# Optimization experiments

Hardware: AMD Instinct MI355X
Metric: run time of the kernel (lower is better)

## Reference

```python
import jax, jax.numpy as jnp
import numpy as np

B, S, D, H = 2, 2048, 1024, 16
HD = D // H  # 64

def setup_inputs() -> dict:
    key = jax.random.key(0)
    ks = jax.random.split(key, 11)
    s = 1.0 / np.sqrt(D)
    inp = {
        "q": jax.random.normal(ks[0], (B, S, D), jnp.float32),
        "k": jax.random.normal(ks[1], (B, S, D), jnp.float32),
        "v": jax.random.normal(ks[2], (B, S, D), jnp.float32),
        "Wq": jax.random.normal(ks[3], (D, D), jnp.float32) * s,
        "bq": jnp.zeros((D,), jnp.float32),
        "Wk": jax.random.normal(ks[4], (D, D), jnp.float32) * s,
        "bk": jnp.zeros((D,), jnp.float32),
        "Wv": jax.random.normal(ks[5], (D, D), jnp.float32) * s,
        "bv": jnp.zeros((D,), jnp.float32),
        "Wo": jax.random.normal(ks[6], (D, D), jnp.float32) * s,
        "bo": jnp.zeros((D,), jnp.float32),
    }
    return inp

def _split_heads(x):
    # [B,S,D] -> [B,H,S,HD]
    b = x.shape[0]
    return x.reshape(b, -1, H, HD).transpose(0, 2, 1, 3)

def reference(q, k, v, Wq, bq, Wk, bk, Wv, bv, Wo, bo):
    qh = _split_heads(q @ Wq.T + bq)
    kh = _split_heads(k @ Wk.T + bk)
    vh = _split_heads(v @ Wv.T + bv)
    scale = 1.0 / jnp.sqrt(jnp.asarray(HD, qh.dtype))
    scores = jnp.einsum("bhqd,bhkd->bhqk", qh, kh) * scale  # [B,H,S,S]
    atten = jax.nn.softmax(scores, axis=-1)  # dropout is eval-mode no-op
    ctx = jnp.einsum("bhqk,bhkd->bhqd", atten, vh)
    out = ctx.transpose(0, 2, 1, 3).reshape(q.shape[0], -1, D)
    return out @ Wo.T + bo, atten
```

## Files before the change

kernel.cpp:

```cpp
#include <hip/hip_runtime.h>
#include <cstdint>

#define B_ 2
#define S_ 2048
#define D_ 1024
#define H_ 16

typedef __bf16 bf16x8 __attribute__((ext_vector_type(8)));
typedef float  f32x4  __attribute__((ext_vector_type(4)));

__device__ __forceinline__ void g2l16(const void* g, void* l) {
  auto* gp = reinterpret_cast<const __attribute__((address_space(1))) uint32_t*>(
      reinterpret_cast<uintptr_t>(g));
  auto* lp = reinterpret_cast<__attribute__((address_space(3))) uint32_t*>(
      reinterpret_cast<uintptr_t>(l));
  __builtin_amdgcn_global_load_lds(gp, lp, 16, 0, 0);
}

__device__ __forceinline__ float exp2_hw(float x) {
#if __has_builtin(__builtin_amdgcn_exp2f)
  return __builtin_amdgcn_exp2f(x);
#else
  return __exp2f(x);
#endif
}

struct CvtArgs {
  const float* s[7];
  __bf16* d[7];
  int n[7];
};

__global__ __launch_bounds__(256) void k_cvt(CvtArgs a) {
  int t = blockIdx.y;
  long i = (long)blockIdx.x * blockDim.x + threadIdx.x;
  long base = i * 8;
  if (base >= a.n[t]) return;
  const float4* sp = (const float4*)(a.s[t] + base);
  float4 x = sp[0], y = sp[1];
  bf16x8 o;
  o[0] = (__bf16)x.x; o[1] = (__bf16)x.y; o[2] = (__bf16)x.z; o[3] = (__bf16)x.w;
  o[4] = (__bf16)y.x; o[5] = (__bf16)y.y; o[6] = (__bf16)y.z; o[7] = (__bf16)y.w;
  *(bf16x8*)(a.d[t] + base) = o;
}

__global__ __launch_bounds__(256, 3) void k_proj(
    const __bf16* __restrict__ Xq, const __bf16* __restrict__ Xk, const __bf16* __restrict__ Xv,
    const __bf16* __restrict__ Wq, const __bf16* __restrict__ Wk, const __bf16* __restrict__ Wv,
    const float* __restrict__ bq, const float* __restrict__ bk, const float* __restrict__ bv,
    __bf16* __restrict__ Oq, __bf16* __restrict__ Ok, __bf16* __restrict__ Ov)
{
  int z = blockIdx.z;
  const __bf16* X = (z == 0) ? Xq : (z == 1) ? Xk : Xv;
  const __bf16* W = (z == 0) ? Wq : (z == 1) ? Wk : Wv;
  const float* bias = (z == 0) ? bq : (z == 1) ? bk : bv;
  __bf16* O = (z == 0) ? Oq : (z == 1) ? Ok : Ov;
  float scale = (z == 0) ? 0.180336880111183f : 1.0f;

  __shared__ bf16x8 As[3][512];
  __shared__ bf16x8 Bs[3][512];

  int t = threadIdx.x, lane = t & 63, w = t >> 6;
  int l15 = lane & 15, l4 = lane >> 4;
  int wr = w >> 1, wc = w & 1;
  int m0 = blockIdx.y * 128, n0 = blockIdx.x * 128;

  int srow = t >> 2, sc = t & 3;
  int ldsoff = __builtin_amdgcn_readfirstlane(w * 1024);
  const __bf16* Xs = X + (size_t)(m0 + srow) * 1024 + sc * 8;
  const __bf16* Wsp = W + (size_t)(n0 + srow) * 1024 + sc * 8;

#define PSTAGE(buf, kt)                                                        \
  {                                                                            \
    _Pragma("unroll")                                                          \
    for (int i = 0; i < 2; ++i) {                                              \
      int lo = __builtin_amdgcn_readfirstlane(i * 4096 + ldsoff);              \
      g2l16(Xs + (size_t)i * 64 * 1024 + (kt) * 32, (char*)As[buf] + lo);      \
      g2l16(Wsp + (size_t)i * 64 * 1024 + (kt) * 32, (char*)Bs[buf] + lo);     \
    }                                                                          \
  }

  f32x4 acc[4][4] = {};

  PSTAGE(0, 0)
  PSTAGE(1, 1)
  asm volatile("s_waitcnt vmcnt(4)" ::: "memory");
  __builtin_amdgcn_s_barrier();
  __builtin_amdgcn_sched_barrier(0);

  int ring = 0;
  for (int kt = 0; kt < 32; ++kt) {
    int cur = ring;
    int rp2 = (ring == 0) ? 2 : ring - 1;
    if (kt + 2 < 32) PSTAGE(rp2, kt + 2)
    __builtin_amdgcn_sched_barrier(0);

    bf16x8 af[4], bfr[4];
#pragma unroll
    for (int i = 0; i < 4; ++i) af[i] = As[cur][(wr * 64 + i * 16 + l15) * 4 + l4];
#pragma unroll
    for (int j = 0; j < 4; ++j) bfr[j] = Bs[cur][(wc * 64 + j * 16 + l15) * 4 + l4];
#pragma unroll
    for (int i = 0; i < 4; ++i)
#pragma unroll
      for (int j = 0; j < 4; ++j)
        acc[i][j] = __builtin_amdgcn_mfma_f32_16x16x32_bf16(af[i], bfr[j], acc[i][j], 0, 0, 0);

    if (kt < 30) {
      asm volatile("s_waitcnt vmcnt(4)" ::: "memory");
      __builtin_amdgcn_s_barrier();
      __builtin_amdgcn_sched_barrier(0);
    } else if (kt == 30) {
      asm volatile("s_waitcnt vmcnt(0)" ::: "memory");
      __builtin_amdgcn_s_barrier();
      __builtin_amdgcn_sched_barrier(0);
    }
    ring = (ring == 2) ? 0 : ring + 1;
  }
#undef PSTAGE

#pragma unroll
  for (int j = 0; j < 4; ++j) {
    int col = n0 + wc * 64 + j * 16 + l15;
    float bv_ = bias[col];
    int h = col >> 6, hd = col & 63;
#pragma unroll
    for (int i = 0; i < 4; ++i) {
#pragma unroll
      for (int r = 0; r < 4; ++r) {
        int row = m0 + wr * 64 + i * 16 + l4 * 4 + r;
        int b = row >> 11, ss = row & 2047;
        float val = (acc[i][j][r] + bv_) * scale;
        O[(((size_t)b * H_ + h) * S_ + ss) * 64 + hd] = (__bf16)val;
      }
    }
  }
}

__global__ __launch_bounds__(256) void k_trans(const __bf16* __restrict__ Vh,
                                               __bf16* __restrict__ VhT)
{
  __shared__ __bf16 Tt[64][72];
  int bid = blockIdx.x;
  int bh = bid >> 5, st = bid & 31;
  int t = threadIdx.x;
  int sr = t >> 2, dc = (t & 3) * 16;
  const __bf16* src = Vh + (((size_t)bh * S_) + st * 64 + sr) * 64 + dc;
  *(bf16x8*)&Tt[sr][dc] = *(const bf16x8*)src;
  *(bf16x8*)&Tt[sr][dc + 8] = *(const bf16x8*)(src + 8);
  __syncthreads();
  int dr = t >> 2, s0 = (t & 3) * 16;
  bf16x8 o0, o1;
#pragma unroll
  for (int ii = 0; ii < 8; ++ii) { o0[ii] = Tt[s0 + ii][dr]; o1[ii] = Tt[s0 + 8 + ii][dr]; }
  __bf16* dst = VhT + ((size_t)bh * 64 + dr) * S_ + st * 64 + s0;
  *(bf16x8*)dst = o0;
  *(bf16x8*)(dst + 8) = o1;
}

__global__ __launch_bounds__(512, 4) void k_attn(
    const __bf16* __restrict__ Qh, const __bf16* __restrict__ Kh,
    const __bf16* __restrict__ VhT, float* __restrict__ atten,
    __bf16* __restrict__ ctxb)
{
  __shared__ bf16x8 KVl[3][1024];
  __shared__ bf16x8 Pl[8 * 176];

  int bid = blockIdx.x;
  int sb = (bid & 7) * 64 + (bid >> 3);
  int bh = sb >> 4, qt = sb & 15;
  int t = threadIdx.x, lane = t & 63, w = t >> 6;
  int l15 = lane & 15, l4 = lane >> 4;
  int q0 = qt * 128 + w * 16;

  const __bf16* Qp = Qh + ((size_t)bh * S_ + q0) * 64;
  bf16x8 qf0 = *(const bf16x8*)(Qp + (size_t)l15 * 64 + l4 * 8);
  bf16x8 qf1 = *(const bf16x8*)(Qp + (size_t)l15 * 64 + 32 + l4 * 8);

  int srow = t >> 3, sc8 = t & 7;
  int scs = sc8 ^ (srow & 7);
  int wbase = __builtin_amdgcn_readfirstlane(w * 1024);

  const __bf16* KpS = Kh + (size_t)bh * S_ * 64 + (size_t)srow * 64 + scs * 8;
  const __bf16* VpS = VhT + (size_t)bh * 64 * S_ + (size_t)srow * S_ + scs * 8;

  float l_part[4] = {0.f, 0.f, 0.f, 0.f};

#define ASTAGE(buf, kt)                                                        \
  {                                                                            \
    g2l16(KpS + (size_t)(kt) * 8192, (char*)KVl[buf] + wbase);                 \
    g2l16(KpS + (size_t)(kt) * 8192 + 4096, (char*)KVl[buf] + 8192 + wbase);   \
  }

  ASTAGE(0, 0)
  ASTAGE(1, 1)
  asm volatile("s_waitcnt vmcnt(2)" ::: "memory");
  __builtin_amdgcn_s_barrier();
  __builtin_amdgcn_sched_barrier(0);

  {
    int ring = 0;
    for (int kt = 0; kt < 16; ++kt) {
      int cur = ring;
      int rp2 = (ring == 0) ? 2 : ring - 1;
      if (kt + 2 < 16) ASTAGE(rp2, kt + 2)
      __builtin_amdgcn_sched_barrier(0);

#pragma unroll
      for (int t8 = 0; t8 < 8; ++t8) {
        int kr = t8 * 16 + l15;
        bf16x8 kf0 = KVl[cur][kr * 8 + ((l4) ^ (kr & 7))];
        bf16x8 kf1 = KVl[cur][kr * 8 + ((4 + l4) ^ (kr & 7))];
        f32x4 a_ = {0.f, 0.f, 0.f, 0.f};
        a_ = __builtin_amdgcn_mfma_f32_16x16x32_bf16(qf0, kf0, a_, 0, 0, 0);
        a_ = __builtin_amdgcn_mfma_f32_16x16x32_bf16(qf1, kf1, a_, 0, 0, 0);
#pragma unroll
        for (int r = 0; r < 4; ++r) l_part[r] += exp2_hw(a_[r]);
      }

      if (kt < 14) {
        asm volatile("s_waitcnt vmcnt(2)" ::: "memory");
        __builtin_amdgcn_s_barrier();
        __builtin_amdgcn_sched_barrier(0);
      } else if (kt == 14) {
        asm volatile("s_waitcnt vmcnt(0)" ::: "memory");
        __builtin_amdgcn_s_barrier();
        __builtin_amdgcn_sched_barrier(0);
      }
      ring = (ring == 2) ? 0 : ring + 1;
    }
  }
#undef ASTAGE

  float inv_l[4];
#pragma unroll
  for (int r = 0; r < 4; ++r) {
    float l = l_part[r];
    l += __shfl_xor(l, 1);
    l += __shfl_xor(l, 2);
    l += __shfl_xor(l, 4);
    l += __shfl_xor(l, 8);
    inv_l[r] = 1.0f / l;
  }

  __builtin_amdgcn_s_barrier();
  __builtin_amdgcn_sched_barrier(0);

  f32x4 ctx[4] = {};
  float* aRow = atten + ((size_t)bh * S_ + q0) * S_;
  __bf16* PlW = (__bf16*)(Pl + w * 176);

#define BSTAGE(buf, kt)                                                        \
  {                                                                            \
    g2l16(KpS + (size_t)(kt) * 4096, (char*)KVl[buf] + wbase);                 \
    g2l16(VpS + (size_t)(kt) * 64, (char*)KVl[buf] + 8192 + wbase);            \
  }

  BSTAGE(0, 0)
  BSTAGE(1, 1)
  asm volatile("s_waitcnt vmcnt(2)" ::: "memory");
  __builtin_amdgcn_s_barrier();
  __builtin_amdgcn_sched_barrier(0);

  {
    int ring = 0;
    for (int kt = 0; kt < 32; ++kt) {
      int cur = ring;
      int rp2 = (ring == 0) ? 2 : ring - 1;
      if (kt + 2 < 32) BSTAGE(rp2, kt + 2)
      __builtin_amdgcn_sched_barrier(0);

      f32x4 sc[4];
#pragma unroll
      for (int t8 = 0; t8 < 4; ++t8) {
        int kr = t8 * 16 + l15;
        bf16x8 kf0 = KVl[cur][kr * 8 + ((l4) ^ (kr & 7))];
        bf16x8 kf1 = KVl[cur][kr * 8 + ((4 + l4) ^ (kr & 7))];
        f32x4 a_ = {0.f, 0.f, 0.f, 0.f};
        a_ = __builtin_amdgcn_mfma_f32_16x16x32_bf16(qf0, kf0, a_, 0, 0, 0);
        a_ = __builtin_amdgcn_mfma_f32_16x16x32_bf16(qf1, kf1, a_, 0, 0, 0);
        sc[t8] = a_;
      }

#pragma unroll
      for (int t8 = 0; t8 < 4; ++t8) {
#pragma unroll
        for (int r = 0; r < 4; ++r) {
          float p = exp2_hw(sc[t8][r]) * inv_l[r];
          __builtin_nontemporal_store(
              p, &aRow[(size_t)(l4 * 4 + r) * S_ + kt * 64 + t8 * 16 + l15]);
          PlW[(l4 * 4 + r) * 88 + t8 * 16 + l15] = (__bf16)p;
        }
      }

#pragma unroll
      for (int kc = 0; kc < 2; ++kc) {
        bf16x8 pa = Pl[w * 176 + l15 * 11 + kc * 4 + l4];
#pragma unroll
        for (int dt = 0; dt < 4; ++dt) {
          int vr = dt * 16 + l15;
          bf16x8 vf = KVl[cur][512 + vr * 8 + ((kc * 4 + l4) ^ (vr & 7))];
          ctx[dt] = __builtin_amdgcn_mfma_f32_16x16x32_bf16(pa, vf, ctx[dt], 0, 0, 0);
        }
      }

      if (kt < 31) {
        asm volatile("s_waitcnt vmcnt(18)" ::: "memory");
        __builtin_amdgcn_s_barrier();
        __builtin_amdgcn_sched_barrier(0);
      }
      ring = (ring == 2) ? 0 : ring + 1;
    }
  }
#undef BSTAGE

  int b = bh >> 4, h = bh & 15;
#pragma unroll
  for (int dt = 0; dt < 4; ++dt) {
#pragma unroll
    for (int r = 0; r < 4; ++r) {
      size_t row = (size_t)b * S_ + q0 + l4 * 4 + r;
      ctxb[row * D_ + h * 64 + dt * 16 + l15] = (__bf16)ctx[dt][r];
    }
  }
}

__global__ __launch_bounds__(256, 3) void k_out(
    const __bf16* __restrict__ X, const __bf16* __restrict__ W,
    const float* __restrict__ bias, float* __restrict__ O)
{
  __shared__ bf16x8 As[3][512];
  __shared__ bf16x8 Bs[3][512];

  int t = threadIdx.x, lane = t & 63, w = t >> 6;
  int l15 = lane & 15, l4 = lane >> 4;
  int wr = w >> 1, wc = w & 1;
  int m0 = blockIdx.y * 128, n0 = blockIdx.x * 128;

  int srow = t >> 2, sc = t & 3;
  int ldsoff = __builtin_amdgcn_readfirstlane(w * 1024);
  const __bf16* Xs = X + (size_t)(m0 + srow) * 1024 + sc * 8;
  const __bf16* Wsp = W + (size_t)(n0 + srow) * 1024 + sc * 8;

#define PSTAGE(buf, kt)                                                        \
  {                                                                            \
    _Pragma("unroll")                                                          \
    for (int i = 0; i < 2; ++i) {                                              \
      int lo = __builtin_amdgcn_readfirstlane(i * 4096 + ldsoff);              \
      g2l16(Xs + (size_t)i * 64 * 1024 + (kt) * 32, (char*)As[buf] + lo);      \
      g2l16(Wsp + (size_t)i * 64 * 1024 + (kt) * 32, (char*)Bs[buf] + lo);     \
    }                                                                          \
  }

  f32x4 acc[4][4] = {};

  PSTAGE(0, 0)
  PSTAGE(1, 1)
  asm volatile("s_waitcnt vmcnt(4)" ::: "memory");
  __builtin_amdgcn_s_barrier();
  __builtin_amdgcn_sched_barrier(0);

  int ring = 0;
  for (int kt = 0; kt < 32; ++kt) {
    int cur = ring;
    int rp2 = (ring == 0) ? 2 : ring - 1;
    if (kt + 2 < 32) PSTAGE(rp2, kt + 2)
    __builtin_amdgcn_sched_barrier(0);

    bf16x8 af[4], bfr[4];
#pragma unroll
    for (int i = 0; i < 4; ++i) af[i] = As[cur][(wr * 64 + i * 16 + l15) * 4 + l4];
#pragma unroll
    for (int j = 0; j < 4; ++j) bfr[j] = Bs[cur][(wc * 64 + j * 16 + l15) * 4 + l4];
#pragma unroll
    for (int i = 0; i < 4; ++i)
#pragma unroll
      for (int j = 0; j < 4; ++j)
        acc[i][j] = __builtin_amdgcn_mfma_f32_16x16x32_bf16(af[i], bfr[j], acc[i][j], 0, 0, 0);

    if (kt < 30) {
      asm volatile("s_waitcnt vmcnt(4)" ::: "memory");
      __builtin_amdgcn_s_barrier();
      __builtin_amdgcn_sched_barrier(0);
    } else if (kt == 30) {
      asm volatile("s_waitcnt vmcnt(0)" ::: "memory");
      __builtin_amdgcn_s_barrier();
      __builtin_amdgcn_sched_barrier(0);
    }
    ring = (ring == 2) ? 0 : ring + 1;
  }
#undef PSTAGE

#pragma unroll
  for (int j = 0; j < 4; ++j) {
    int col = n0 + wc * 64 + j * 16 + l15;
    float bv_ = bias[col];
#pragma unroll
    for (int i = 0; i < 4; ++i) {
#pragma unroll
      for (int r = 0; r < 4; ++r) {
        int row = m0 + wr * 64 + i * 16 + l4 * 4 + r;
        __builtin_nontemporal_store(acc[i][j][r] + bv_, &O[(size_t)row * 1024 + col]);
      }
    }
  }
}

extern "C" void kernel_launch(void* const* d_in, const int* in_sizes, int n_in,
                              void* d_out, int out_size, void* d_ws, size_t ws_size,
                              hipStream_t stream)
{
  const float* q  = (const float*)d_in[0];
  const float* k  = (const float*)d_in[1];
  const float* v  = (const float*)d_in[2];
  const float* Wq = (const float*)d_in[3];
  const float* bq = (const float*)d_in[4];
  const float* Wk = (const float*)d_in[5];
  const float* bk = (const float*)d_in[6];
  const float* Wv = (const float*)d_in[7];
  const float* bv = (const float*)d_in[8];
  const float* Wo = (const float*)d_in[9];
  const float* bo = (const float*)d_in[10];

  const size_t NBSD = (size_t)B_ * S_ * D_;
  const size_t NDD  = (size_t)D_ * D_;

  float* out = (float*)d_out;
  float* atten = out + NBSD;

  if (ws_size < 2 * (NBSD * 4 + NDD * 4 + NBSD * 4)) return;

  __bf16* ws = (__bf16*)d_ws;
  __bf16* qb  = ws;
  __bf16* kb  = ws + NBSD;
  __bf16* vb  = ws + 2 * NBSD;
  __bf16* Wqb = ws + 3 * NBSD;
  __bf16* Wkb = Wqb + NDD;
  __bf16* Wvb = Wkb + NDD;
  __bf16* Wob = Wvb + NDD;
  __bf16* Qh  = Wob + NDD;
  __bf16* Kh  = Qh + NBSD;
  __bf16* Vh  = Kh + NBSD;
  __bf16* VhT = Vh + NBSD;
  __bf16* ctxb = qb;

  CvtArgs ca;
  ca.s[0] = q;  ca.d[0] = qb;  ca.n[0] = (int)NBSD;
  ca.s[1] = k;  ca.d[1] = kb;  ca.n[1] = (int)NBSD;
  ca.s[2] = v;  ca.d[2] = vb;  ca.n[2] = (int)NBSD;
  ca.s[3] = Wq; ca.d[3] = Wqb; ca.n[3] = (int)NDD;
  ca.s[4] = Wk; ca.d[4] = Wkb; ca.n[4] = (int)NDD;
  ca.s[5] = Wv; ca.d[5] = Wvb; ca.n[5] = (int)NDD;
  ca.s[6] = Wo; ca.d[6] = Wob; ca.n[6] = (int)NDD;

  k_cvt<<<dim3(2048, 7), 256, 0, stream>>>(ca);
  k_proj<<<dim3(8, 32, 3), 256, 0, stream>>>(qb, kb, vb, Wqb, Wkb, Wvb,
                                             bq, bk, bv, Qh, Kh, Vh);
  k_trans<<<dim3(1024), 256, 0, stream>>>(Vh, VhT);
  k_attn<<<dim3(512), 512, 0, stream>>>(Qh, Kh, VhT, atten, ctxb);
  k_out<<<dim3(8, 32), 256, 0, stream>>>(ctxb, Wob, bo, out);
}
```

Measured before the change: 274.1 us.

## Transpose MFMA score layout to vectorize attention and P stores, reorder prefetch

Swaps the MFMA operands so each lane holds four consecutive key columns of one query row instead of four rows. This lets the large attention-probability write become 16-byte vector stores, and the bf16 P tile go to LDS as 8-byte stores. The row-sum reduction becomes a two-step cross-lane shuffle. It also moves the K/V prefetch after the compute with a retuned vmcnt wait, and drops the nontemporal hint on the output-projection stores. The hand-counted vmcnt values now depend on how many stores are in flight, so an incorrect count risks reading K/V tiles before they arrive.

```diff
diff --git a/kernel.cpp b/kernel.cpp
--- a/kernel.cpp
+++ b/kernel.cpp
@@ -7,6 +7,7 @@
 #define H_ 16
 
 typedef __bf16 bf16x8 __attribute__((ext_vector_type(8)));
+typedef __bf16 bf16x4 __attribute__((ext_vector_type(4)));
 typedef float  f32x4  __attribute__((ext_vector_type(4)));
 
 __device__ __forceinline__ void g2l16(const void* g, void* l) {
@@ -184,7 +185,7 @@
   const __bf16* KpS = Kh + (size_t)bh * S_ * 64 + (size_t)srow * 64 + scs * 8;
   const __bf16* VpS = VhT + (size_t)bh * 64 * S_ + (size_t)srow * S_ + scs * 8;
 
-  float l_part[4] = {0.f, 0.f, 0.f, 0.f};
+  float l_part = 0.f;
 
 #define ASTAGE(buf, kt)                                                        \
   {                                                                            \
@@ -212,10 +213,10 @@
         bf16x8 kf0 = KVl[cur][kr * 8 + ((l4) ^ (kr & 7))];
         bf16x8 kf1 = KVl[cur][kr * 8 + ((4 + l4) ^ (kr & 7))];
         f32x4 a_ = {0.f, 0.f, 0.f, 0.f};
-        a_ = __builtin_amdgcn_mfma_f32_16x16x32_bf16(qf0, kf0, a_, 0, 0, 0);
-        a_ = __builtin_amdgcn_mfma_f32_16x16x32_bf16(qf1, kf1, a_, 0, 0, 0);
-#pragma unroll
-        for (int r = 0; r < 4; ++r) l_part[r] += exp2_hw(a_[r]);
+        a_ = __builtin_amdgcn_mfma_f32_16x16x32_bf16(kf0, qf0, a_, 0, 0, 0);
+        a_ = __builtin_amdgcn_mfma_f32_16x16x32_bf16(kf1, qf1, a_, 0, 0, 0);
+#pragma unroll
+        for (int r = 0; r < 4; ++r) l_part += exp2_hw(a_[r]);
       }
 
       if (kt < 14) {
@@ -232,22 +233,19 @@
   }
 #undef ASTAGE
 
-  float inv_l[4];
-#pragma unroll
-  for (int r = 0; r < 4; ++r) {
-    float l = l_part[r];
-    l += __shfl_xor(l, 1);
-    l += __shfl_xor(l, 2);
-    l += __shfl_xor(l, 4);
-    l += __shfl_xor(l, 8);
-    inv_l[r] = 1.0f / l;
+  float inv_l;
+  {
+    float l = l_part;
+    l += __shfl_xor(l, 16);
+    l += __shfl_xor(l, 32);
+    inv_l = 1.0f / l;
   }
 
   __builtin_amdgcn_s_barrier();
   __builtin_amdgcn_sched_barrier(0);
 
   f32x4 ctx[4] = {};
-  float* aRow = atten + ((size_t)bh * S_ + q0) * S_;
+  float* aRowT = atten + ((size_t)bh * S_ + q0 + l15) * S_;
   __bf16* PlW = (__bf16*)(Pl + w * 176);
 
 #define BSTAGE(buf, kt)                                                        \
@@ -267,8 +265,6 @@
     for (int kt = 0; kt < 32; ++kt) {
       int cur = ring;
       int rp2 = (ring == 0) ? 2 : ring - 1;
-      if (kt + 2 < 32) BSTAGE(rp2, kt + 2)
-      __builtin_amdgcn_sched_barrier(0);
 
       f32x4 sc[4];
 #pragma unroll
@@ -277,25 +273,28 @@
         bf16x8 kf0 = KVl[cur][kr * 8 + ((l4) ^ (kr & 7))];
         bf16x8 kf1 = KVl[cur][kr * 8 + ((4 + l4) ^ (kr & 7))];
         f32x4 a_ = {0.f, 0.f, 0.f, 0.f};
-        a_ = __builtin_amdgcn_mfma_f32_16x16x32_bf16(qf0, kf0, a_, 0, 0, 0);
-        a_ = __builtin_amdgcn_mfma_f32_16x16x32_bf16(qf1, kf1, a_, 0, 0, 0);
+        a_ = __builtin_amdgcn_mfma_f32_16x16x32_bf16(kf0, qf0, a_, 0, 0, 0);
+        a_ = __builtin_amdgcn_mfma_f32_16x16x32_bf16(kf1, qf1, a_, 0, 0, 0);
         sc[t8] = a_;
       }
 
 #pragma unroll
       for (int t8 = 0; t8 < 4; ++t8) {
+        f32x4 pv;
+        bf16x4 pb;
 #pragma unroll
         for (int r = 0; r < 4; ++r) {
-          float p = exp2_hw(sc[t8][r]) * inv_l[r];
-          __builtin_nontemporal_store(
-              p, &aRow[(size_t)(l4 * 4 + r) * S_ + kt * 64 + t8 * 16 + l15]);
-          PlW[(l4 * 4 + r) * 88 + t8 * 16 + l15] = (__bf16)p;
+          float p = exp2_hw(sc[t8][r]) * inv_l;
+          pv[r] = p;
+          pb[r] = (__bf16)p;
         }
+        *(f32x4*)(aRowT + kt * 64 + t8 * 16 + l4 * 4) = pv;
+        *(bf16x4*)(PlW + l15 * 88 + t8 * 16 + l4 * 4) = pb;
       }
 
 #pragma unroll
       for (int kc = 0; kc < 2; ++kc) {
-        bf16x8 pa = Pl[w * 176 + l15 * 11 + kc * 4 + l4];
+        bf16x8 pa = *(const bf16x8*)(PlW + l15 * 88 + kc * 32 + l4 * 8);
 #pragma unroll
         for (int dt = 0; dt < 4; ++dt) {
           int vr = dt * 16 + l15;
@@ -304,8 +303,16 @@
         }
       }
 
-      if (kt < 31) {
-        asm volatile("s_waitcnt vmcnt(18)" ::: "memory");
+      __builtin_amdgcn_sched_barrier(0);
+      if (kt + 2 < 32) BSTAGE(rp2, kt + 2)
+      __builtin_amdgcn_sched_barrier(0);
+
+      if (kt < 30) {
+        asm volatile("s_waitcnt vmcnt(10)" ::: "memory");
+        __builtin_amdgcn_s_barrier();
+        __builtin_amdgcn_sched_barrier(0);
+      } else if (kt == 30) {
+        asm volatile("s_waitcnt vmcnt(4)" ::: "memory");
         __builtin_amdgcn_s_barrier();
         __builtin_amdgcn_sched_barrier(0);
       }
@@ -400,7 +407,7 @@
 #pragma unroll
       for (int r = 0; r < 4; ++r) {
         int row = m0 + wr * 64 + i * 16 + l4 * 4 + r;
-        __builtin_nontemporal_store(acc[i][j][r] + bv_, &O[(size_t)row * 1024 + col]);
+        O[(size_t)row * 1024 + col] = acc[i][j][r] + bv_;
       }
     }
   }
```

After: 292.1 us. 1.07x slower.
